# Kernel optimization log

Hardware: AMD Instinct MI355X
Metric: run time of the kernel (lower is better)

Reference implementation:

```python
import jax, jax.numpy as jnp
import numpy as np

N = 100000          # nodes
E = 1600000         # edges (avg degree 16)
IN = 128            # in_channels
OUT = 64            # out_channels
HID = 2 * OUT       # first GCN layer width per Encoder (non-skip)


def setup_inputs() -> dict:
    key = jax.random.key(0)
    k0, k1, k2, k3 = jax.random.split(key, 4)
    x = jax.random.normal(k0, (N, IN), dtype=jnp.float32)
    edge_index = jax.random.randint(k1, (2, E), 0, N, dtype=jnp.int32)
    W1 = jax.random.normal(k2, (IN, HID), dtype=jnp.float32) / np.float32(np.sqrt(IN))
    b1 = jnp.zeros((HID,), jnp.float32)
    W2 = jax.random.normal(k3, (HID, OUT), dtype=jnp.float32) / np.float32(np.sqrt(HID))
    b2 = jnp.zeros((OUT,), jnp.float32)
    a = jnp.float32(0.25)  # PReLU slope (single shared parameter)
    return {"x": x, "edge_index": edge_index, "W1": W1, "b1": b1, "W2": W2, "b2": b2, "a": a}


def _gcn_layer(x, W, b, src, dst, n):
    # GCNConv: h = x W; symmetric normalization with self-loops already in src/dst
    h = x @ W                                                   # [N, F]
    deg = jax.ops.segment_sum(jnp.ones_like(dst, dtype=h.dtype), dst, num_segments=n)
    dinv = jnp.where(deg > 0, jax.lax.rsqrt(deg), jnp.float32(0.0))
    norm = dinv[src] * dinv[dst]                                # [E']
    msg = h[src] * norm[:, None]                                # gather + scale
    return jax.ops.segment_sum(msg, dst, num_segments=n) + b    # scatter-sum


def _prelu(x, a):
    return jnp.where(x >= 0, x, a * x)


def reference(x, edge_index, W1, b1, W2, b2, a):
    n = x.shape[0]
    loops = jnp.arange(n, dtype=edge_index.dtype)
    src = jnp.concatenate([edge_index[0], loops])   # add self-loops (GCNConv default)
    dst = jnp.concatenate([edge_index[1], loops])
    h = _prelu(_gcn_layer(x, W1, b1, src, dst, n), a)
    return _prelu(_gcn_layer(h, W2, b2, src, dst, n), a)
```

## Files before the change

### kernel.cpp

```cpp
#include <hip/hip_runtime.h>


#define THREADS 256
#define SCAN_CHUNK 1024
#define NBLK  128
#define BINSH 7
#define BINSZ 128
#define KMAX  1024

typedef unsigned short bf16_t;
typedef __attribute__((ext_vector_type(8))) short bf16x8;
typedef __attribute__((ext_vector_type(4))) float f32x4;

__device__ __forceinline__ float bflo(unsigned int w) {
    union { unsigned int u; float f; } v; v.u = w << 16; return v.f;
}
__device__ __forceinline__ float bfhi(unsigned int w) {
    union { unsigned int u; float f; } v; v.u = w & 0xffff0000u; return v.f;
}
__device__ __forceinline__ unsigned int f2bf(float f) {
    union { float f; unsigned int u; } v; v.f = f;
    return (v.u + 0x7fffu + ((v.u >> 16) & 1u)) >> 16;
}

__global__ __launch_bounds__(THREADS) void hist_kernel(const int* __restrict__ dst,
                                                       int* __restrict__ hist,
                                                       int e, int K, int chunk) {
    __shared__ int h[KMAX];
    int t = threadIdx.x, b = blockIdx.x;
    for (int i = t; i < K; i += THREADS) h[i] = 0;
    __syncthreads();
    int lo = b * chunk, hi = min(lo + chunk, e);
    for (int i = lo + t; i < hi; i += THREADS) atomicAdd(&h[dst[i] >> BINSH], 1);
    __syncthreads();
    for (int i = t; i < K; i += THREADS) hist[i * NBLK + b] = h[i];
}

__global__ void scan_phaseA_kernel(const int* __restrict__ in, int* __restrict__ bsum, int m) {
    __shared__ int sdata[256];
    int base = blockIdx.x * SCAN_CHUNK;
    int t = threadIdx.x;
    int s = 0;
#pragma unroll
    for (int k = 0; k < 4; ++k) {
        int idx = base + t * 4 + k;
        if (idx < m) s += in[idx];
    }
    sdata[t] = s;
    __syncthreads();
    for (int d = 128; d > 0; d >>= 1) {
        if (t < d) sdata[t] += sdata[t + d];
        __syncthreads();
    }
    if (t == 0) bsum[blockIdx.x] = sdata[0];
}

__global__ void scan_phaseB_kernel(int* __restrict__ bsum, int nb) {
    __shared__ int sdata[256];
    __shared__ int carry;
    int t = threadIdx.x;
    if (t == 0) carry = 0;
    __syncthreads();
    for (int base = 0; base < nb; base += 256) {
        int idx = base + t;
        int v = (idx < nb) ? bsum[idx] : 0;
        sdata[t] = v;
        __syncthreads();
        for (int d = 1; d < 256; d <<= 1) {
            int u = (t >= d) ? sdata[t - d] : 0;
            __syncthreads();
            sdata[t] += u;
            __syncthreads();
        }
        int excl = sdata[t] - v + carry;
        if (idx < nb) bsum[idx] = excl;
        int tot = sdata[255];
        __syncthreads();
        if (t == 0) carry += tot;
        __syncthreads();
    }
}

__global__ void scan_phaseC_kernel(const int* __restrict__ in, const int* __restrict__ bsum,
                                   int* __restrict__ outx, int m) {
    __shared__ int sdata[256];
    int base = blockIdx.x * SCAN_CHUNK;
    int t = threadIdx.x;
    int v[4];
    int s = 0;
#pragma unroll
    for (int k = 0; k < 4; ++k) {
        int idx = base + t * 4 + k;
        v[k] = (idx < m) ? in[idx] : 0;
        s += v[k];
    }
    sdata[t] = s;
    __syncthreads();
    for (int d = 1; d < 256; d <<= 1) {
        int u = (t >= d) ? sdata[t - d] : 0;
        __syncthreads();
        sdata[t] += u;
        __syncthreads();
    }
    int run = bsum[blockIdx.x] + sdata[t] - s;
#pragma unroll
    for (int k = 0; k < 4; ++k) {
        int idx = base + t * 4 + k;
        if (idx < m) { outx[idx] = run; run += v[k]; }
    }
}

__global__ __launch_bounds__(THREADS) void rank_scatter_kernel(const int* __restrict__ src,
                                                               const int* __restrict__ dst,
                                                               const int* __restrict__ hoff,
                                                               unsigned int* __restrict__ sorted,
                                                               int e, int K, int chunk) {
    __shared__ int cntl[KMAX];
    __shared__ int basel[KMAX];
    int t = threadIdx.x, b = blockIdx.x;
    for (int i = t; i < K; i += THREADS) { cntl[i] = 0; basel[i] = hoff[i * NBLK + b]; }
    __syncthreads();
    int lo = b * chunk, hi = min(lo + chunk, e);
    for (int i = lo + t; i < hi; i += THREADS) {
        int d = dst[i];
        int bin = d >> BINSH;
        int r = atomicAdd(&cntl[bin], 1);
        sorted[basel[bin] + r] = (unsigned int)src[i] | ((unsigned int)(d & (BINSZ - 1)) << 25);
    }
}

__global__ __launch_bounds__(THREADS) void bin_build_kernel(const unsigned int* __restrict__ sorted,
                                                            const int* __restrict__ hoff,
                                                            float* __restrict__ dinv,
                                                            int* __restrict__ off,
                                                            int* __restrict__ cnt,
                                                            int* __restrict__ es,
                                                            int n, int e, int K) {
    __shared__ int scnt[BINSZ];
    __shared__ int soff[BINSZ];
    int b = blockIdx.x, t = threadIdx.x;
    int base = hoff[b * NBLK];
    int end  = (b + 1 < K) ? hoff[(b + 1) * NBLK] : e;
    int m = end - base;
    if (t < BINSZ) scnt[t] = 0;
    __syncthreads();
    for (int i = t; i < m; i += THREADS) atomicAdd(&scnt[sorted[base + i] >> 25], 1);
    __syncthreads();
    if (t < BINSZ) soff[t] = scnt[t];
    __syncthreads();
    for (int d = 1; d < BINSZ; d <<= 1) {
        int v = (t < BINSZ && t >= d) ? soff[t - d] : 0;
        __syncthreads();
        if (t < BINSZ) soff[t] += v;
        __syncthreads();
    }
    if (t < BINSZ) {
        int ex = soff[t] - scnt[t];
        int node = (b << BINSH) + t;
        if (node < n) {
            off[node]  = base + ex;
            cnt[node]  = scnt[t];
            dinv[node] = rsqrtf((float)(scnt[t] + 1));
        }
        soff[t] = ex;
    }
    __syncthreads();
    for (int i = t; i < m; i += THREADS) {
        unsigned int pk = sorted[base + i];
        int pos = atomicAdd(&soff[pk >> 25], 1);
        es[base + pos] = (int)(pk & 0x01FFFFFFu);
    }
}

__global__ void wt_kernel(const float* __restrict__ W, bf16_t* __restrict__ WT,
                          int Kdim, int C) {
    int tid = blockIdx.x * blockDim.x + threadIdx.x;
    if (tid >= Kdim * C) return;
    int c = tid / Kdim, k = tid % Kdim;
    WT[(size_t)c * Kdim + k] = (bf16_t)f2bf(W[(size_t)k * C + c]);
}

template <int OUTC, bool XBF>
__global__ __launch_bounds__(THREADS) void gemm_mfma_kernel(const void* __restrict__ Xv,
                                                            const bf16_t* __restrict__ WT,
                                                            const float* __restrict__ rowscale,
                                                            bf16_t* __restrict__ H, int n) {
    constexpr int CT = OUTC / 16;
    int wid  = (int)threadIdx.x >> 6;
    int lane = (int)threadIdx.x & 63;
    int rbase = blockIdx.x * 64 + wid * 16;
    int col16 = lane & 15;
    int kgrp  = lane >> 4;

    int rowA = rbase + col16;
    if (rowA >= n) rowA = n - 1;

    bf16x8 a[4];
#pragma unroll
    for (int ks = 0; ks < 4; ++ks) {
        int kb = ks * 32 + kgrp * 8;
        if constexpr (XBF) {
            a[ks] = *reinterpret_cast<const bf16x8*>((const bf16_t*)Xv + (size_t)rowA * 128 + kb);
        } else {
            const float* xp = (const float*)Xv + (size_t)rowA * 128 + kb;
            float4 x0 = *reinterpret_cast<const float4*>(xp);
            float4 x1 = *reinterpret_cast<const float4*>(xp + 4);
            bf16x8 t;
            t[0] = (short)f2bf(x0.x); t[1] = (short)f2bf(x0.y);
            t[2] = (short)f2bf(x0.z); t[3] = (short)f2bf(x0.w);
            t[4] = (short)f2bf(x1.x); t[5] = (short)f2bf(x1.y);
            t[6] = (short)f2bf(x1.z); t[7] = (short)f2bf(x1.w);
            a[ks] = t;
        }
    }

    int r0 = rbase + kgrp * 4;
    float sc[4];
#pragma unroll
    for (int j = 0; j < 4; ++j) sc[j] = (r0 + j < n) ? rowscale[r0 + j] : 0.f;

#pragma unroll
    for (int ct = 0; ct < CT; ++ct) {
        const bf16_t* wp = WT + (size_t)(ct * 16 + col16) * 128 + kgrp * 8;
        f32x4 acc = {0.f, 0.f, 0.f, 0.f};
#pragma unroll
        for (int ks = 0; ks < 4; ++ks) {
            bf16x8 b = *reinterpret_cast<const bf16x8*>(wp + ks * 32);
            acc = __builtin_amdgcn_mfma_f32_16x16x32_bf16(a[ks], b, acc, 0, 0, 0);
        }
#pragma unroll
        for (int j = 0; j < 4; ++j) {
            int r = r0 + j;
            if (r < n) H[(size_t)r * OUTC + ct * 16 + col16] = (bf16_t)f2bf(acc[j] * sc[j]);
        }
    }
}

template <int F, bool OUTBF>
__global__ __launch_bounds__(THREADS) void agg_kernel(const bf16_t* __restrict__ H,
                                                      const float* __restrict__ dinv,
                                                      const int* __restrict__ off,
                                                      const int* __restrict__ cnt,
                                                      const int* __restrict__ es,
                                                      const float* __restrict__ bias,
                                                      const float* __restrict__ a_ptr,
                                                      void* __restrict__ outv, int n) {
    constexpr int TPN = F / 8;
    int node = blockIdx.x * (THREADS / TPN) + (int)threadIdx.x / TPN;
    int l8   = (int)threadIdx.x % TPN;
    if (node >= n) return;
    const int fbase = l8 * 8;

    float acc[8];
    {
        uint4 v = *reinterpret_cast<const uint4*>(H + (size_t)node * F + fbase);
        acc[0] = bflo(v.x); acc[1] = bfhi(v.x);
        acc[2] = bflo(v.y); acc[3] = bfhi(v.y);
        acc[4] = bflo(v.z); acc[5] = bfhi(v.z);
        acc[6] = bflo(v.w); acc[7] = bfhi(v.w);
    }

    int j0 = off[node];
    int m  = cnt[node];
    int i = 0;
    for (; i + 3 < m; i += 4) {
        int s0 = es[j0 + i], s1 = es[j0 + i + 1], s2 = es[j0 + i + 2], s3 = es[j0 + i + 3];
        uint4 v0 = *reinterpret_cast<const uint4*>(H + (size_t)s0 * F + fbase);
        uint4 v1 = *reinterpret_cast<const uint4*>(H + (size_t)s1 * F + fbase);
        uint4 v2 = *reinterpret_cast<const uint4*>(H + (size_t)s2 * F + fbase);
        uint4 v3 = *reinterpret_cast<const uint4*>(H + (size_t)s3 * F + fbase);
        acc[0] += (bflo(v0.x) + bflo(v1.x)) + (bflo(v2.x) + bflo(v3.x));
        acc[1] += (bfhi(v0.x) + bfhi(v1.x)) + (bfhi(v2.x) + bfhi(v3.x));
        acc[2] += (bflo(v0.y) + bflo(v1.y)) + (bflo(v2.y) + bflo(v3.y));
        acc[3] += (bfhi(v0.y) + bfhi(v1.y)) + (bfhi(v2.y) + bfhi(v3.y));
        acc[4] += (bflo(v0.z) + bflo(v1.z)) + (bflo(v2.z) + bflo(v3.z));
        acc[5] += (bfhi(v0.z) + bfhi(v1.z)) + (bfhi(v2.z) + bfhi(v3.z));
        acc[6] += (bflo(v0.w) + bflo(v1.w)) + (bflo(v2.w) + bflo(v3.w));
        acc[7] += (bfhi(v0.w) + bfhi(v1.w)) + (bfhi(v2.w) + bfhi(v3.w));
    }
    for (; i < m; ++i) {
        int s0 = es[j0 + i];
        uint4 v0 = *reinterpret_cast<const uint4*>(H + (size_t)s0 * F + fbase);
        acc[0] += bflo(v0.x); acc[1] += bfhi(v0.x);
        acc[2] += bflo(v0.y); acc[3] += bfhi(v0.y);
        acc[4] += bflo(v0.z); acc[5] += bfhi(v0.z);
        acc[6] += bflo(v0.w); acc[7] += bfhi(v0.w);
    }

    float di = dinv[node];
    float a  = *a_ptr;
    float4 b0 = *reinterpret_cast<const float4*>(bias + fbase);
    float4 b1 = *reinterpret_cast<const float4*>(bias + fbase + 4);
    float bb[8] = {b0.x, b0.y, b0.z, b0.w, b1.x, b1.y, b1.z, b1.w};
    float o[8];
#pragma unroll
    for (int k = 0; k < 8; ++k) {
        float v = acc[k] * di + bb[k];
        o[k] = v >= 0.f ? v : a * v;
    }

    if constexpr (OUTBF) {
        uint4 w;
        w.x = f2bf(o[0]) | (f2bf(o[1]) << 16);
        w.y = f2bf(o[2]) | (f2bf(o[3]) << 16);
        w.z = f2bf(o[4]) | (f2bf(o[5]) << 16);
        w.w = f2bf(o[6]) | (f2bf(o[7]) << 16);
        *reinterpret_cast<uint4*>((bf16_t*)outv + (size_t)node * F + fbase) = w;
    } else {
        float* op = (float*)outv + (size_t)node * F + fbase;
        *reinterpret_cast<float4*>(op)     = make_float4(o[0], o[1], o[2], o[3]);
        *reinterpret_cast<float4*>(op + 4) = make_float4(o[4], o[5], o[6], o[7]);
    }
}

extern "C" void kernel_launch(void* const* d_in, const int* in_sizes, int n_in,
                              void* d_out, int out_size, void* d_ws, size_t ws_size,
                              hipStream_t stream) {
    const float* x   = (const float*)d_in[0];
    const int*   ei  = (const int*)d_in[1];
    const float* W1  = (const float*)d_in[2];
    const float* b1  = (const float*)d_in[3];
    const float* W2  = (const float*)d_in[4];
    const float* b2  = (const float*)d_in[5];
    const float* a   = (const float*)d_in[6];

    const int IN  = 128;
    const int HID = 128;
    const int OUT = 64;
    const int n = in_sizes[0] / IN;
    const int e = in_sizes[1] / 2;
    const int* src = ei;
    const int* dst = ei + e;

    const int K     = (n + BINSZ - 1) >> BINSH;
    const int chunk = (e + NBLK - 1) / NBLK;
    const int M     = K * NBLK;
    const int nb    = (M + SCAN_CHUNK - 1) / SCAN_CHUNK;

    auto align = [](size_t v) { return (v + 255) / 256 * 256; };
    char* ws = (char*)d_ws;
    size_t o = 0;
    int*          hist   = (int*)(ws + o);          o += align((size_t)M * 4);
    int*          hoff   = (int*)(ws + o);          o += align((size_t)M * 4);
    int*          bsum   = (int*)(ws + o);          o += align((size_t)nb * 4);
    unsigned int* sorted = (unsigned int*)(ws + o); o += align((size_t)e * 4);
    int*          es     = (int*)(ws + o);          o += align((size_t)e * 4);
    float*        dinv   = (float*)(ws + o);        o += align((size_t)n * 4);
    int*          off    = (int*)(ws + o);          o += align((size_t)n * 4);
    int*          cnt    = (int*)(ws + o);          o += align((size_t)n * 4);
    bf16_t*       h1     = (bf16_t*)(ws + o);       o += align((size_t)n * HID * 2);
    bf16_t*       h2     = (bf16_t*)(ws + o);       o += align((size_t)n * HID * 2);
    bf16_t*       g      = (bf16_t*)(ws + o);       o += align((size_t)n * OUT * 2);
    bf16_t*       WT1    = (bf16_t*)(ws + o);       o += align((size_t)IN * HID * 2);
    bf16_t*       WT2    = (bf16_t*)(ws + o);       o += align((size_t)HID * OUT * 2);

    float* out = (float*)d_out;

    wt_kernel<<<(IN * HID + THREADS - 1) / THREADS, THREADS, 0, stream>>>(W1, WT1, IN, HID);
    wt_kernel<<<(HID * OUT + THREADS - 1) / THREADS, THREADS, 0, stream>>>(W2, WT2, HID, OUT);

    hist_kernel<<<NBLK, THREADS, 0, stream>>>(dst, hist, e, K, chunk);
    scan_phaseA_kernel<<<nb, THREADS, 0, stream>>>(hist, bsum, M);
    scan_phaseB_kernel<<<1, THREADS, 0, stream>>>(bsum, nb);
    scan_phaseC_kernel<<<nb, THREADS, 0, stream>>>(hist, bsum, hoff, M);
    rank_scatter_kernel<<<NBLK, THREADS, 0, stream>>>(src, dst, hoff, sorted, e, K, chunk);
    bin_build_kernel<<<K, THREADS, 0, stream>>>(sorted, hoff, dinv, off, cnt, es, n, e, K);

    int gbG = (n + 63) / 64;

    gemm_mfma_kernel<128, false><<<gbG, THREADS, 0, stream>>>(x, WT1, dinv, h1, n);
    {
        constexpr int NPB = THREADS / (128 / 8);
        int gb = (n + NPB - 1) / NPB;
        agg_kernel<128, true><<<gb, THREADS, 0, stream>>>(h1, dinv, off, cnt, es, b1, a, h2, n);
    }

    gemm_mfma_kernel<64, true><<<gbG, THREADS, 0, stream>>>(h2, WT2, dinv, g, n);
    {
        constexpr int NPB = THREADS / (64 / 8);
        int gb = (n + NPB - 1) / NPB;
        agg_kernel<64, false><<<gb, THREADS, 0, stream>>>(g, dinv, off, cnt, es, b2, a, out, n);
    }

    (void)ws_size; (void)n_in; (void)out_size;
}
```

Before: 227.5 us.

## Split layer-1 features into two 64-wide halves for cache-friendlier aggregation

The first GEMM now writes its 128-wide output as two separate 64-column buffers. The layer-1 aggregation runs twice over those halves, so each gather pass touches a smaller working set that fits better in L2/MALL. The second GEMM reads the split input back. The two weight-transpose kernels are merged into one launch, and the histogram/scatter block count is doubled. The cost is an extra pass over the edge list and index reads, plus one more kernel launch.

```diff
diff --git a/kernel.cpp b/kernel.cpp
--- a/kernel.cpp
+++ b/kernel.cpp
@@ -3,7 +3,7 @@
 
 #define THREADS 256
 #define SCAN_CHUNK 1024
-#define NBLK  128
+#define NBLK  256
 #define BINSH 7
 #define BINSZ 128
 #define KMAX  1024
@@ -172,19 +172,28 @@
     }
 }
 
-__global__ void wt_kernel(const float* __restrict__ W, bf16_t* __restrict__ WT,
-                          int Kdim, int C) {
+__global__ void wt2_kernel(const float* __restrict__ W1, bf16_t* __restrict__ WT1,
+                           const float* __restrict__ W2, bf16_t* __restrict__ WT2,
+                           int K1, int C1, int K2, int C2) {
     int tid = blockIdx.x * blockDim.x + threadIdx.x;
-    if (tid >= Kdim * C) return;
-    int c = tid / Kdim, k = tid % Kdim;
-    WT[(size_t)c * Kdim + k] = (bf16_t)f2bf(W[(size_t)k * C + c]);
-}
-
-template <int OUTC, bool XBF>
+    int t1 = K1 * C1;
+    if (tid < t1) {
+        int c = tid / K1, k = tid % K1;
+        WT1[(size_t)c * K1 + k] = (bf16_t)f2bf(W1[(size_t)k * C1 + c]);
+    } else if (tid < t1 + K2 * C2) {
+        int id = tid - t1;
+        int c = id / K2, k = id % K2;
+        WT2[(size_t)c * K2 + k] = (bf16_t)f2bf(W2[(size_t)k * C2 + c]);
+    }
+}
+
+template <int OUTC, bool XBF, bool XSPLIT, bool OSPLIT>
 __global__ __launch_bounds__(THREADS) void gemm_mfma_kernel(const void* __restrict__ Xv,
+                                                            const void* __restrict__ Xv2,
                                                             const bf16_t* __restrict__ WT,
                                                             const float* __restrict__ rowscale,
-                                                            bf16_t* __restrict__ H, int n) {
+                                                            bf16_t* __restrict__ H,
+                                                            bf16_t* __restrict__ H2, int n) {
     constexpr int CT = OUTC / 16;
     int wid  = (int)threadIdx.x >> 6;
     int lane = (int)threadIdx.x & 63;
@@ -200,7 +209,12 @@
     for (int ks = 0; ks < 4; ++ks) {
         int kb = ks * 32 + kgrp * 8;
         if constexpr (XBF) {
-            a[ks] = *reinterpret_cast<const bf16x8*>((const bf16_t*)Xv + (size_t)rowA * 128 + kb);
+            if constexpr (XSPLIT) {
+                const bf16_t* xb = (ks < 2) ? (const bf16_t*)Xv : (const bf16_t*)Xv2;
+                a[ks] = *reinterpret_cast<const bf16x8*>(xb + (size_t)rowA * 64 + (kb & 63));
+            } else {
+                a[ks] = *reinterpret_cast<const bf16x8*>((const bf16_t*)Xv + (size_t)rowA * 128 + kb);
+            }
         } else {
             const float* xp = (const float*)Xv + (size_t)rowA * 128 + kb;
             float4 x0 = *reinterpret_cast<const float4*>(xp);
@@ -231,7 +245,15 @@
 #pragma unroll
         for (int j = 0; j < 4; ++j) {
             int r = r0 + j;
-            if (r < n) H[(size_t)r * OUTC + ct * 16 + col16] = (bf16_t)f2bf(acc[j] * sc[j]);
+            if (r < n) {
+                bf16_t val = (bf16_t)f2bf(acc[j] * sc[j]);
+                if constexpr (OSPLIT) {
+                    if (ct < CT / 2) H [(size_t)r * (OUTC / 2) + ct * 16 + col16] = val;
+                    else             H2[(size_t)r * (OUTC / 2) + (ct - CT / 2) * 16 + col16] = val;
+                } else {
+                    H[(size_t)r * OUTC + ct * 16 + col16] = val;
+                }
+            }
         }
     }
 }
@@ -348,16 +370,21 @@
     float*        dinv   = (float*)(ws + o);        o += align((size_t)n * 4);
     int*          off    = (int*)(ws + o);          o += align((size_t)n * 4);
     int*          cnt    = (int*)(ws + o);          o += align((size_t)n * 4);
-    bf16_t*       h1     = (bf16_t*)(ws + o);       o += align((size_t)n * HID * 2);
-    bf16_t*       h2     = (bf16_t*)(ws + o);       o += align((size_t)n * HID * 2);
+    bf16_t*       h1a    = (bf16_t*)(ws + o);       o += align((size_t)n * 64 * 2);
+    bf16_t*       h1b    = (bf16_t*)(ws + o);       o += align((size_t)n * 64 * 2);
+    bf16_t*       h2a    = (bf16_t*)(ws + o);       o += align((size_t)n * 64 * 2);
+    bf16_t*       h2b    = (bf16_t*)(ws + o);       o += align((size_t)n * 64 * 2);
     bf16_t*       g      = (bf16_t*)(ws + o);       o += align((size_t)n * OUT * 2);
     bf16_t*       WT1    = (bf16_t*)(ws + o);       o += align((size_t)IN * HID * 2);
     bf16_t*       WT2    = (bf16_t*)(ws + o);       o += align((size_t)HID * OUT * 2);
 
     float* out = (float*)d_out;
 
-    wt_kernel<<<(IN * HID + THREADS - 1) / THREADS, THREADS, 0, stream>>>(W1, WT1, IN, HID);
-    wt_kernel<<<(HID * OUT + THREADS - 1) / THREADS, THREADS, 0, stream>>>(W2, WT2, HID, OUT);
+    {
+        int tot = IN * HID + HID * OUT;
+        wt2_kernel<<<(tot + THREADS - 1) / THREADS, THREADS, 0, stream>>>(
+            W1, WT1, W2, WT2, IN, HID, HID, OUT);
+    }
 
     hist_kernel<<<NBLK, THREADS, 0, stream>>>(dst, hist, e, K, chunk);
     scan_phaseA_kernel<<<nb, THREADS, 0, stream>>>(hist, bsum, M);
@@ -367,20 +394,17 @@
     bin_build_kernel<<<K, THREADS, 0, stream>>>(sorted, hoff, dinv, off, cnt, es, n, e, K);
 
     int gbG = (n + 63) / 64;
-
-    gemm_mfma_kernel<128, false><<<gbG, THREADS, 0, stream>>>(x, WT1, dinv, h1, n);
-    {
-        constexpr int NPB = THREADS / (128 / 8);
-        int gb = (n + NPB - 1) / NPB;
-        agg_kernel<128, true><<<gb, THREADS, 0, stream>>>(h1, dinv, off, cnt, es, b1, a, h2, n);
-    }
-
-    gemm_mfma_kernel<64, true><<<gbG, THREADS, 0, stream>>>(h2, WT2, dinv, g, n);
-    {
-        constexpr int NPB = THREADS / (64 / 8);
-        int gb = (n + NPB - 1) / NPB;
-        agg_kernel<64, false><<<gb, THREADS, 0, stream>>>(g, dinv, off, cnt, es, b2, a, out, n);
-    }
+    constexpr int NPB = THREADS / (64 / 8);
+    int gbA = (n + NPB - 1) / NPB;
+
+    gemm_mfma_kernel<128, false, false, true><<<gbG, THREADS, 0, stream>>>(
+        x, nullptr, WT1, dinv, h1a, h1b, n);
+    agg_kernel<64, true><<<gbA, THREADS, 0, stream>>>(h1a, dinv, off, cnt, es, b1,      a, h2a, n);
+    agg_kernel<64, true><<<gbA, THREADS, 0, stream>>>(h1b, dinv, off, cnt, es, b1 + 64, a, h2b, n);
+
+    gemm_mfma_kernel<64, true, true, false><<<gbG, THREADS, 0, stream>>>(
+        h2a, h2b, WT2, dinv, g, nullptr, n);
+    agg_kernel<64, false><<<gbA, THREADS, 0, stream>>>(g, dinv, off, cnt, es, b2, a, out, n);
 
     (void)ws_size; (void)n_in; (void)out_size;
 }
```

New measurement: 211.0 us. 7.3% less time.
